# Performance work log

Hardware: AMD Instinct MI355X
Metric: run time of the kernel (lower is better)

## Reference

```python
import jax, jax.numpy as jnp
import numpy as np

# Dims: B=batch, C=n_car, N=n_node, E=embed_dim, H=n_heads
B, C, N, E = 64, 8, 512, 512
H = 8
CLIP = 10.0


def setup_inputs() -> dict:
    key = jax.random.key(0)
    ks = jax.random.split(key, 12)
    s = 1.0 / np.sqrt(E)
    mask = jax.random.bernoulli(ks[10], 0.3, (B, C, 1, N))
    mask = mask.at[..., 0].set(False)  # ensure at least one unmasked node per (b,c)
    return {
        "node_embeddings": jax.random.normal(ks[0], (B, N, E), jnp.float32),
        "graph_embedding": jax.random.normal(ks[1], (B, E), jnp.float32),
        "step_context": jax.random.normal(ks[2], (B, C, 1, E + 2), jnp.float32),
        "mask": mask,
        "Wk1": jax.random.normal(ks[3], (E, E), jnp.float32) * s,
        "Wv": jax.random.normal(ks[4], (E, E), jnp.float32) * s,
        "Wk2": jax.random.normal(ks[5], (E, E), jnp.float32) * s,
        "Wq_fixed": jax.random.normal(ks[6], (E, E), jnp.float32) * s,
        "Wout": jax.random.normal(ks[7], (E, E), jnp.float32) * s,
        "Wq_step": jax.random.normal(ks[8], (E, E + 2), jnp.float32) * s,
        "v": jax.random.uniform(ks[9], (E,), jnp.float32, -s, s),
    }


def reference(node_embeddings, graph_embedding, step_context, mask,
              Wk1, Wv, Wk2, Wq_fixed, Wout, Wq_step, v):
    dh = E // H
    neg = jnp.asarray(-1e9, node_embeddings.dtype)

    # compute_static: projections (torch Linear: x @ W.T). K/V/Q_fixed are
    # broadcast over the car dim instead of materialized via .repeat (same math).
    Q_fixed = (graph_embedding @ Wq_fixed.T)[:, None, None, :]  # [B,1,1,E]
    K1 = node_embeddings @ Wk1.T                                 # [B,N,E]
    V = node_embeddings @ Wv.T                                   # [B,N,E]
    K2 = node_embeddings @ Wk2.T                                 # [B,N,E]

    # compute_dynamic
    Q_step = step_context @ Wq_step.T                            # [B,C,1,E]
    Q1 = Q_fixed + Q_step                                        # [B,C,1,E]

    # MHA (need_W=False): split heads, masked scaled dot-product, merge heads.
    qh = Q1.reshape(B, C, H, dh)                                 # q-len 1 squeezed
    kh = K1.reshape(B, N, H, dh)
    vh = V.reshape(B, N, H, dh)
    scores = jnp.einsum('bchd,bnhd->bchn', qh, kh) * (1.0 / np.sqrt(dh))
    m = mask[:, :, 0, :][:, :, None, :]                          # [B,C,1,N]
    scores = jnp.where(m, neg, scores)
    attn = jax.nn.softmax(scores, axis=-1)
    heads = jnp.einsum('bchn,bnhd->bchd', attn, vh).reshape(B, C, E)
    Q3 = heads @ Wout.T                                          # [B,C,E] (Q2.squeeze(2))

    # Pointer logits (SHA): u = tanh(Q_fixed+Q_step) @ v, repeated over E,
    # dotted with K2 => u_scalar * sum_e K2, then tanh-clipped and masked.
    u_scalar = jnp.einsum('bcqe,e->bcq', jnp.tanh(Q1), v)        # [B,C,1]
    k2sum = K2.sum(-1)                                           # [B,N]
    raw = u_scalar * k2sum[:, None, :]                           # [B,C,N]
    logits = CLIP * jnp.tanh(raw * (1.0 / np.sqrt(E)))
    logits = jnp.where(mask[:, :, 0, :], neg, logits)
    logits = logits.reshape(B, C * N)                            # view(batch, -1)
    return logits, Q3
```

## Files before the change

kernel.cpp:

```cpp
#include <hip/hip_runtime.h>


typedef _Float16 f16x8 __attribute__((ext_vector_type(8)));
typedef float f32x4 __attribute__((ext_vector_type(4)));

__device__ __forceinline__ void async16(const void* g, void* l) {
  __builtin_amdgcn_global_load_lds(
      (const __attribute__((address_space(1))) unsigned int*)g,
      (__attribute__((address_space(3))) unsigned int*)l, 16, 0, 0);
}

__global__ __launch_bounds__(256) void prep_w(const float* __restrict__ Wk1,
                                              const float* __restrict__ Wv,
                                              const float* __restrict__ Wk2,
                                              _Float16* __restrict__ W1h,
                                              _Float16* __restrict__ W2h,
                                              float* __restrict__ colsum) {
  const int bid = blockIdx.x;
  if (bid < 16) {
    const int tx = threadIdx.x & 31, ty = threadIdx.x >> 5;
    const int col = bid * 32 + tx;
    float s = 0.f;
#pragma unroll 4
    for (int e = ty * 64; e < ty * 64 + 64; ++e) s += Wk2[e * 512 + col];
    __shared__ float red[8][32];
    red[ty][tx] = s;
    __syncthreads();
    if (ty == 0) {
      float t = 0.f;
#pragma unroll
      for (int g = 0; g < 8; ++g) t += red[g][tx];
      colsum[col] = t;
    }
  } else {
    const int cb = bid - 16;
    const float* src = (cb < 128) ? Wk1 : Wv;
    _Float16* dst = (cb < 128) ? W1h : W2h;
    const size_t off = (size_t)(cb & 127) * 2048 + threadIdx.x * 8;
    float4 a = *(const float4*)(src + off);
    float4 b = *(const float4*)(src + off + 4);
    union { _Float16 h[8]; uint4 u; } pk;
    pk.h[0] = (_Float16)a.x; pk.h[1] = (_Float16)a.y;
    pk.h[2] = (_Float16)a.z; pk.h[3] = (_Float16)a.w;
    pk.h[4] = (_Float16)b.x; pk.h[5] = (_Float16)b.y;
    pk.h[6] = (_Float16)b.z; pk.h[7] = (_Float16)b.w;
    *(uint4*)(dst + off) = pk.u;
  }
}

__global__ __launch_bounds__(256) void q1_mfma_kernel(
    const float* __restrict__ ge, const float* __restrict__ sc,
    const float* __restrict__ Wqf, const float* __restrict__ Wqs,
    float* __restrict__ Q1) {
  const int mb = blockIdx.x, nb = blockIdx.y, ks = blockIdx.z;
  const int tid = threadIdx.x;
  const int lane = tid & 63, wave = tid >> 6;
  const int wm = (wave >> 1) * 32, wn = (wave & 1) * 32;

  __shared__ __align__(16) _Float16 As[64][40];
  __shared__ __align__(16) _Float16 Ws[64][40];

  f32x4 acc[2][2] = {};
  const int qd = (lane >> 4) * 8, rr = lane & 15;

  for (int kt = 0; kt < 9; ++kt) {
    const int kb = ks * 288 + kt * 32;
#pragma unroll
    for (int f0 = 0; f0 < 2; ++f0) {
      int f = tid + f0 * 256;
      int r = f >> 3, c4 = (f & 7) * 4;
      int m = mb * 64 + r;
      int e = nb * 64 + r;
#pragma unroll
      for (int j = 0; j < 4; ++j) {
        int k = kb + c4 + j;
        float a = 0.f, w = 0.f;
        if (k < 512) {
          a = ge[(m >> 3) * 512 + k];
          w = Wqf[(size_t)e * 512 + k];
        } else if (k < 1026) {
          a = sc[(size_t)m * 514 + (k - 512)];
          w = Wqs[(size_t)e * 514 + (k - 512)];
        }
        As[r][c4 + j] = (_Float16)a;
        Ws[r][c4 + j] = (_Float16)w;
      }
    }
    __syncthreads();
    f16x8 af[2], bfr[2];
#pragma unroll
    for (int mi = 0; mi < 2; ++mi) af[mi] = *(const f16x8*)&As[wm + mi * 16 + rr][qd];
#pragma unroll
    for (int ni = 0; ni < 2; ++ni) bfr[ni] = *(const f16x8*)&Ws[wn + ni * 16 + rr][qd];
#pragma unroll
    for (int mi = 0; mi < 2; ++mi)
#pragma unroll
      for (int ni = 0; ni < 2; ++ni)
        acc[mi][ni] =
            __builtin_amdgcn_mfma_f32_16x16x32_f16(af[mi], bfr[ni], acc[mi][ni], 0, 0, 0);
    __syncthreads();
  }

  const int col = lane & 15, rq = (lane >> 4) * 4;
#pragma unroll
  for (int mi = 0; mi < 2; ++mi)
#pragma unroll
    for (int ni = 0; ni < 2; ++ni)
#pragma unroll
      for (int r = 0; r < 4; ++r) {
        int m = mb * 64 + wm + mi * 16 + rq + r;
        int e = nb * 64 + wn + ni * 16 + col;
        atomicAdd(&Q1[(size_t)m * 512 + e], acc[mi][ni][r]);
      }
}

__global__ __launch_bounds__(256, 2) void gemm_kv(
    const float* __restrict__ A, const _Float16* __restrict__ W1,
    const _Float16* __restrict__ W2, const float* __restrict__ colsum,
    _Float16* __restrict__ K1, _Float16* __restrict__ Vt,
    float* __restrict__ k2sum) {
  const int flat = (int)(blockIdx.y * 4 + blockIdx.x);
  const int work = (flat & 7) * 128 + (flat >> 3);
  const int nb = work & 3;
  const int mb = work >> 2;
  const int tid = threadIdx.x, lane = tid & 63, wave = tid >> 6;
  const int wm = (wave >> 1) * 64, wn = (wave & 1) * 64;
  const int row0 = mb * 128, col0 = nb * 128;
  const int b = mb >> 2;

  __shared__ __align__(16) _Float16 Ah[128 * 64];
  __shared__ __align__(16) _Float16 Wb[2][2][128 * 64];

  f32x4 acc1[4][4] = {}, acc2[4][4] = {};
  float k2p[4] = {0.f, 0.f, 0.f, 0.f};
  const int q = lane >> 4, rr = lane & 15;
  const int wlr = lane >> 3, wlc = lane & 7;
  const int cswz = wlc ^ wlr;

  const int ar0 = tid >> 3, ac = tid & 7;
  const float* aptr = A + (size_t)(row0 + ar0) * 512 + ac * 8;
  const int aslot = ac ^ (ar0 & 7);

  float4 areg[4][2];
  float4 cs0, cs1;

  auto issue_a = [&](int kt) {
#pragma unroll
    for (int j = 0; j < 4; ++j) {
      const float* gp = aptr + (size_t)j * 32 * 512 + kt * 64;
      areg[j][0] = *(const float4*)gp;
      areg[j][1] = *(const float4*)(gp + 4);
    }
    if (nb == 0) {
      const float* csp = colsum + kt * 64 + ac * 8;
      cs0 = *(const float4*)csp;
      cs1 = *(const float4*)(csp + 4);
    }
  };
  auto issue_w = [&](int kt, int buf) {
    const int kbase = kt * 64;
#pragma unroll
    for (int j = 0; j < 4; ++j) {
      int r = wave * 32 + j * 8 + wlr;
      int ldsrow = (wave * 32 + j * 8) * 64;
      size_t goff = (size_t)(col0 + r) * 512 + kbase + cswz * 8;
      async16(W1 + goff, &Wb[buf][0][ldsrow]);
      async16(W2 + goff, &Wb[buf][1][ldsrow]);
    }
  };
  auto write_a = [&](int kt) {
#pragma unroll
    for (int j = 0; j < 4; ++j) {
      union { _Float16 h[8]; uint4 u; } pk;
      float4 lo = areg[j][0], hi = areg[j][1];
      pk.h[0] = (_Float16)lo.x; pk.h[1] = (_Float16)lo.y;
      pk.h[2] = (_Float16)lo.z; pk.h[3] = (_Float16)lo.w;
      pk.h[4] = (_Float16)hi.x; pk.h[5] = (_Float16)hi.y;
      pk.h[6] = (_Float16)hi.z; pk.h[7] = (_Float16)hi.w;
      *(uint4*)&Ah[(ar0 + 32 * j) * 64 + aslot * 8] = pk.u;
    }
    if (nb == 0) {
#pragma unroll
      for (int j = 0; j < 4; ++j) {
        float4 lo = areg[j][0], hi = areg[j][1];
        k2p[j] += lo.x * cs0.x + lo.y * cs0.y + lo.z * cs0.z + lo.w * cs0.w +
                  hi.x * cs1.x + hi.y * cs1.y + hi.z * cs1.z + hi.w * cs1.w;
      }
    }
  };

  issue_a(0);
  issue_w(0, 0);
  write_a(0);
  __syncthreads();

  for (int kt = 0; kt < 8; ++kt) {
    const int p = kt & 1;
    if (kt < 7) {
      issue_a(kt + 1);
      issue_w(kt + 1, p ^ 1);
    }
#pragma unroll
    for (int k0 = 0; k0 < 64; k0 += 32) {
      const int cb = (k0 >> 3) + q;
      f16x8 af[4], b1[4], b2[4];
#pragma unroll
      for (int mi = 0; mi < 4; ++mi) {
        int ra = wm + mi * 16 + rr;
        af[mi] = *(const f16x8*)&Ah[ra * 64 + (cb ^ (ra & 7)) * 8];
      }
#pragma unroll
      for (int ni = 0; ni < 4; ++ni) {
        int rw = wn + ni * 16 + rr;
        int slot = cb ^ (rw & 7);
        b1[ni] = *(const f16x8*)&Wb[p][0][rw * 64 + slot * 8];
        b2[ni] = *(const f16x8*)&Wb[p][1][rw * 64 + slot * 8];
      }
      __builtin_amdgcn_s_setprio(1);
#pragma unroll
      for (int mi = 0; mi < 4; ++mi)
#pragma unroll
        for (int ni = 0; ni < 4; ++ni) {
          acc1[mi][ni] =
              __builtin_amdgcn_mfma_f32_16x16x32_f16(af[mi], b1[ni], acc1[mi][ni], 0, 0, 0);
          acc2[mi][ni] =
              __builtin_amdgcn_mfma_f32_16x16x32_f16(af[mi], b2[ni], acc2[mi][ni], 0, 0, 0);
        }
      __builtin_amdgcn_s_setprio(0);
    }
    if (kt < 7) {
      __syncthreads();
      write_a(kt + 1);
      __syncthreads();
    }
  }

  if (nb == 0) {
#pragma unroll
    for (int j = 0; j < 4; ++j) {
      float s = k2p[j];
      s += __shfl_xor(s, 1, 8);
      s += __shfl_xor(s, 2, 8);
      s += __shfl_xor(s, 4, 8);
      if (ac == 0) k2sum[row0 + ar0 + 32 * j] = s;
    }
  }

  const int col = lane & 15, rq = (lane >> 4) * 4;
#pragma unroll
  for (int mi = 0; mi < 4; ++mi)
#pragma unroll
    for (int ni = 0; ni < 4; ++ni)
#pragma unroll
      for (int r = 0; r < 4; ++r) {
        size_t m = row0 + wm + mi * 16 + rq + r;
        size_t e = col0 + wn + ni * 16 + col;
        K1[m * 512 + e] = (_Float16)acc1[mi][ni][r];
      }

  _Float16* Vts = &Wb[0][0][0];
#pragma unroll
  for (int mi = 0; mi < 4; ++mi)
#pragma unroll
    for (int ni = 0; ni < 4; ++ni) {
      int n0 = wm + mi * 16 + rq;
      int el = wn + ni * 16 + col;
      int cn = n0 >> 3, half = (n0 >> 2) & 1;
      int slot = cn ^ (el & 7);
      union { _Float16 h[4]; unsigned long long u; } pk;
#pragma unroll
      for (int r = 0; r < 4; ++r) pk.h[r] = (_Float16)acc2[mi][ni][r];
      *(unsigned long long*)&Vts[el * 128 + slot * 8 + half * 4] = pk.u;
    }
  __syncthreads();
  const int nbase = row0 & 511;
#pragma unroll
  for (int i = 0; i < 8; ++i) {
    int f = tid + i * 256;
    int el = f >> 4, c16 = f & 15;
    int slot = c16 ^ (el & 7);
    uint4 val = *(const uint4*)&Vts[el * 128 + slot * 8];
    *(uint4*)(Vt + (size_t)b * 262144 + (size_t)(col0 + el) * 512 + nbase + c16 * 8) = val;
  }
}

__global__ __launch_bounds__(256) void attn_kernel(
    const float* __restrict__ Q1, const _Float16* __restrict__ K1,
    const _Float16* __restrict__ Vt, const int* __restrict__ mask,
    float* __restrict__ heads) {
  const int bid = blockIdx.x;
  const int b = bid >> 3, h = bid & 7;
  const int tid = threadIdx.x, wave = tid >> 6, lane = tid & 63;
  const int q = lane >> 4, cl = lane & 15;

  __shared__ __align__(16) _Float16 kt[256 * 64];
  __shared__ __align__(16) _Float16 P[16][520];
  __shared__ float red[4][8];

  f16x8 af[2];
  {
    const float* qp = Q1 + (size_t)(b * 8 + (cl & 7)) * 512 + h * 64 + q * 8;
#pragma unroll
    for (int s = 0; s < 2; ++s) {
      float4 l0 = *(const float4*)(qp + s * 32);
      float4 l1 = *(const float4*)(qp + s * 32 + 4);
      af[s][0] = (_Float16)l0.x; af[s][1] = (_Float16)l0.y;
      af[s][2] = (_Float16)l0.z; af[s][3] = (_Float16)l0.w;
      af[s][4] = (_Float16)l1.x; af[s][5] = (_Float16)l1.y;
      af[s][6] = (_Float16)l1.z; af[s][7] = (_Float16)l1.w;
    }
  }

  f32x4 acc[8] = {};
  const _Float16* Kb = K1 + (size_t)b * 262144 + h * 64;
  for (int h2 = 0; h2 < 2; ++h2) {
#pragma unroll
    for (int j = 0; j < 8; ++j) {
      int r = wave * 64 + j * 8 + (lane >> 3);
      int cg = (lane & 7) ^ (r & 7);
      async16(Kb + (size_t)(h2 * 256 + r) * 512 + cg * 8, &kt[(wave * 64 + j * 8) * 64]);
    }
    __syncthreads();
    __builtin_amdgcn_s_setprio(1);
#pragma unroll
    for (int tt = 0; tt < 4; ++tt) {
      int rn = wave * 64 + tt * 16 + cl;
#pragma unroll
      for (int s = 0; s < 2; ++s) {
        int slot = (s * 4 + q) ^ (cl & 7);
        f16x8 bf = *(const f16x8*)&kt[rn * 64 + slot * 8];
        acc[h2 * 4 + tt] =
            __builtin_amdgcn_mfma_f32_16x16x32_f16(af[s], bf, acc[h2 * 4 + tt], 0, 0, 0);
      }
    }
    __builtin_amdgcn_s_setprio(0);
    __syncthreads();
  }

  const _Float16* Vb = Vt + (size_t)b * 262144 + (size_t)h * 64 * 512;
#pragma unroll
  for (int j = 0; j < 8; ++j) {
    int r = wave * 16 + j * 2 + (lane >> 5);
    int cg = (lane & 31) ^ (r & 7);
    async16(Vb + (size_t)r * 512 + cg * 8, &kt[(wave * 16 + j * 2) * 256]);
  }

  float gmax[4], rsum[4];
  if (q < 2) {
    float mx[4] = {-3e38f, -3e38f, -3e38f, -3e38f};
#pragma unroll
    for (int t = 0; t < 8; ++t) {
      int n = (t >> 2) * 256 + wave * 64 + (t & 3) * 16 + cl;
#pragma unroll
      for (int r = 0; r < 4; ++r) {
        int c = q * 4 + r;
        float x = mask[(size_t)(b * 8 + c) * 512 + n] ? -1e9f : acc[t][r] * 0.125f;
        acc[t][r] = x;
        mx[r] = fmaxf(mx[r], x);
      }
    }
#pragma unroll
    for (int off = 1; off < 16; off <<= 1)
#pragma unroll
      for (int r = 0; r < 4; ++r) mx[r] = fmaxf(mx[r], __shfl_xor(mx[r], off, 64));
    if (cl == 0)
#pragma unroll
      for (int r = 0; r < 4; ++r) red[wave][q * 4 + r] = mx[r];
  }
  __syncthreads();
  if (q < 2) {
#pragma unroll
    for (int r = 0; r < 4; ++r) {
      int c = q * 4 + r;
      gmax[r] = fmaxf(fmaxf(red[0][c], red[1][c]), fmaxf(red[2][c], red[3][c]));
    }
  }
  __syncthreads();
  if (q < 2) {
#pragma unroll
    for (int r = 0; r < 4; ++r) rsum[r] = 0.f;
#pragma unroll
    for (int t = 0; t < 8; ++t) {
      int n = (t >> 2) * 256 + wave * 64 + (t & 3) * 16 + cl;
#pragma unroll
      for (int r = 0; r < 4; ++r) {
        float e = __expf(acc[t][r] - gmax[r]);
        rsum[r] += e;
        P[q * 4 + r][n] = (_Float16)e;
      }
    }
#pragma unroll
    for (int off = 1; off < 16; off <<= 1)
#pragma unroll
      for (int r = 0; r < 4; ++r) rsum[r] += __shfl_xor(rsum[r], off, 64);
    if (cl == 0)
#pragma unroll
      for (int r = 0; r < 4; ++r) red[wave][q * 4 + r] = rsum[r];
  }
  __syncthreads();

  f32x4 pacc = {};
  const int rn = wave * 16 + cl;
  __builtin_amdgcn_s_setprio(1);
#pragma unroll
  for (int sl = 0; sl < 8; ++sl) {
    int slot = (sl * 4 + q) ^ (cl & 7);
    f16x8 bf = *(const f16x8*)&kt[rn * 256 + slot * 8];
    f16x8 pa = *(const f16x8*)&P[cl][sl * 32 + q * 8];
    pacc = __builtin_amdgcn_mfma_f32_16x16x32_f16(pa, bf, pacc, 0, 0, 0);
  }
  __builtin_amdgcn_s_setprio(0);
  __syncthreads();
#pragma unroll
  for (int j = 0; j < 8; ++j) {
    int r = wave * 16 + j * 2 + (lane >> 5);
    int cg = (lane & 31) ^ (r & 7);
    async16(Vb + (size_t)r * 512 + 256 + cg * 8, &kt[(wave * 16 + j * 2) * 256]);
  }
  __syncthreads();
  __builtin_amdgcn_s_setprio(1);
#pragma unroll
  for (int sl = 0; sl < 8; ++sl) {
    int slot = (sl * 4 + q) ^ (cl & 7);
    f16x8 bf = *(const f16x8*)&kt[rn * 256 + slot * 8];
    f16x8 pa = *(const f16x8*)&P[cl][256 + sl * 32 + q * 8];
    pacc = __builtin_amdgcn_mfma_f32_16x16x32_f16(pa, bf, pacc, 0, 0, 0);
  }
  __builtin_amdgcn_s_setprio(0);

  if (q < 2) {
#pragma unroll
    for (int r = 0; r < 4; ++r) {
      int c = q * 4 + r;
      float inv = 1.f / (red[0][c] + red[1][c] + red[2][c] + red[3][c]);
      heads[(size_t)(b * 8 + c) * 512 + h * 64 + wave * 16 + cl] = pacc[r] * inv;
    }
  }
}

__global__ __launch_bounds__(256) void gemm_out64(const float* __restrict__ A,
                                                  const float* __restrict__ W,
                                                  float* __restrict__ C) {
  const int mb = blockIdx.x, nb = blockIdx.y, ks = blockIdx.z;
  const int tid = threadIdx.x;
  const int lane = tid & 63, wave = tid >> 6;
  const int wm = (wave >> 1) * 32, wn = (wave & 1) * 32;

  __shared__ __align__(16) _Float16 As[64][40];
  __shared__ __align__(16) _Float16 Ws[64][40];

  f32x4 acc[2][2] = {};
  const int qd = (lane >> 4) * 8, rr = lane & 15;

  for (int kt = 0; kt < 8; ++kt) {
    const int kb = ks * 256 + kt * 32;
#pragma unroll
    for (int f0 = 0; f0 < 2; ++f0) {
      int f = tid + f0 * 256;
      int r = f >> 3, c4 = (f & 7) * 4;
      float4 a = *(const float4*)(A + (size_t)(mb * 64 + r) * 512 + kb + c4);
      float4 w = *(const float4*)(W + (size_t)(nb * 64 + r) * 512 + kb + c4);
      As[r][c4 + 0] = (_Float16)a.x; As[r][c4 + 1] = (_Float16)a.y;
      As[r][c4 + 2] = (_Float16)a.z; As[r][c4 + 3] = (_Float16)a.w;
      Ws[r][c4 + 0] = (_Float16)w.x; Ws[r][c4 + 1] = (_Float16)w.y;
      Ws[r][c4 + 2] = (_Float16)w.z; Ws[r][c4 + 3] = (_Float16)w.w;
    }
    __syncthreads();
    f16x8 af[2], bfr[2];
#pragma unroll
    for (int mi = 0; mi < 2; ++mi) af[mi] = *(const f16x8*)&As[wm + mi * 16 + rr][qd];
#pragma unroll
    for (int ni = 0; ni < 2; ++ni) bfr[ni] = *(const f16x8*)&Ws[wn + ni * 16 + rr][qd];
#pragma unroll
    for (int mi = 0; mi < 2; ++mi)
#pragma unroll
      for (int ni = 0; ni < 2; ++ni)
        acc[mi][ni] =
            __builtin_amdgcn_mfma_f32_16x16x32_f16(af[mi], bfr[ni], acc[mi][ni], 0, 0, 0);
    __syncthreads();
  }

  const int col = lane & 15, rq = (lane >> 4) * 4;
#pragma unroll
  for (int mi = 0; mi < 2; ++mi)
#pragma unroll
    for (int ni = 0; ni < 2; ++ni)
#pragma unroll
      for (int r = 0; r < 4; ++r) {
        int m = mb * 64 + wm + mi * 16 + rq + r;
        int e = nb * 64 + wn + ni * 16 + col;
        atomicAdd(&C[(size_t)m * 512 + e], acc[mi][ni][r]);
      }
}

__global__ __launch_bounds__(256) void logits_u_kernel(
    const float* __restrict__ Q1, const float* __restrict__ v,
    const float* __restrict__ k2s, const int* __restrict__ mask,
    float* __restrict__ out) {
  const int bc = blockIdx.x;
  const int b = bc >> 3;
  const int tid = threadIdx.x;
  const int wave = tid >> 6, lane = tid & 63;

  float p = tanhf(Q1[(size_t)bc * 512 + tid]) * v[tid] +
            tanhf(Q1[(size_t)bc * 512 + tid + 256]) * v[tid + 256];
#pragma unroll
  for (int off = 32; off; off >>= 1) p += __shfl_down(p, off, 64);
  __shared__ float red[4];
  __shared__ float su;
  if (lane == 0) red[wave] = p;
  __syncthreads();
  if (tid == 0) su = red[0] + red[1] + red[2] + red[3];
  __syncthreads();
  const float u = su;

#pragma unroll
  for (int i = 0; i < 2; ++i) {
    int n = tid + i * 256;
    int idx = bc * 512 + n;
    out[idx] = mask[idx] ? -1e9f
                         : 10.f * tanhf(u * k2s[b * 512 + n] * 0.04419417382415922f);
  }
}

extern "C" void kernel_launch(void* const* d_in, const int* in_sizes, int n_in,
                              void* d_out, int out_size, void* d_ws, size_t ws_size,
                              hipStream_t stream) {
  const float* ne = (const float*)d_in[0];
  const float* ge = (const float*)d_in[1];
  const float* sc = (const float*)d_in[2];
  const int* mask = (const int*)d_in[3];
  const float* Wk1 = (const float*)d_in[4];
  const float* Wv = (const float*)d_in[5];
  const float* Wk2 = (const float*)d_in[6];
  const float* Wqf = (const float*)d_in[7];
  const float* Wout = (const float*)d_in[8];
  const float* Wqs = (const float*)d_in[9];
  const float* v = (const float*)d_in[10];

  float* logits = (float*)d_out;
  float* q3 = (float*)d_out + 262144;

  char* ws = (char*)d_ws;
  _Float16* K1 = (_Float16*)(ws + 0);
  _Float16* Vt = (_Float16*)(ws + 33554432);
  float* Q1 = (float*)(ws + 67108864);
  float* heads = (float*)(ws + 68157440);
  float* k2sum = (float*)(ws + 69206016);
  float* colsum = (float*)(ws + 69337088);
  _Float16* W1h = (_Float16*)(ws + 69339136);
  _Float16* W2h = (_Float16*)(ws + 69863424);

  hipMemsetAsync(Q1, 0, 1048576, stream);
  hipMemsetAsync(q3, 0, 1048576, stream);
  prep_w<<<272, 256, 0, stream>>>(Wk1, Wv, Wk2, W1h, W2h, colsum);
  q1_mfma_kernel<<<dim3(8, 8, 4), 256, 0, stream>>>(ge, sc, Wqf, Wqs, Q1);
  gemm_kv<<<dim3(4, 256), 256, 0, stream>>>(ne, W1h, W2h, colsum, K1, Vt, k2sum);
  attn_kernel<<<512, 256, 0, stream>>>(Q1, K1, Vt, mask, heads);
  gemm_out64<<<dim3(8, 8, 2), 256, 0, stream>>>(heads, Wout, q3);
  logits_u_kernel<<<512, 256, 0, stream>>>(Q1, v, k2sum, mask, logits);
}
```

Before: 216.8 us.

## Split fused K1/V GEMM into separate passes to raise occupancy

The fused gemm_kv kernel, which computed K1 and V together from one shared A tile, is split into two block types, each computing a single output (K1 or V). This halves the accumulator registers and the W shared-memory buffers per block, and launch bounds rise to 3 blocks per CU, with 2048 blocks instead of 1024. In exchange, each A tile is now loaded from global memory and converted to fp16 twice, once per pass. The k2sum reduction moves to only the pass-0 nb-0 blocks.

```diff
diff --git a/kernel.cpp b/kernel.cpp
--- a/kernel.cpp
+++ b/kernel.cpp
@@ -114,24 +114,29 @@
       }
 }
 
-__global__ __launch_bounds__(256, 2) void gemm_kv(
+__global__ __launch_bounds__(256, 3) void gemm_kv(
     const float* __restrict__ A, const _Float16* __restrict__ W1,
     const _Float16* __restrict__ W2, const float* __restrict__ colsum,
     _Float16* __restrict__ K1, _Float16* __restrict__ Vt,
     float* __restrict__ k2sum) {
-  const int flat = (int)(blockIdx.y * 4 + blockIdx.x);
-  const int work = (flat & 7) * 128 + (flat >> 3);
+  const int flat = (int)blockIdx.x;
+  const int work = (flat & 7) * 256 + (flat >> 3);
+  const int mb = work >> 3;
+  const int pass = (work >> 2) & 1;
   const int nb = work & 3;
-  const int mb = work >> 2;
+  const bool do_k2 = (work & 7) == 0;
   const int tid = threadIdx.x, lane = tid & 63, wave = tid >> 6;
   const int wm = (wave >> 1) * 64, wn = (wave & 1) * 64;
   const int row0 = mb * 128, col0 = nb * 128;
   const int b = mb >> 2;
 
-  __shared__ __align__(16) _Float16 Ah[128 * 64];
-  __shared__ __align__(16) _Float16 Wb[2][2][128 * 64];
-
-  f32x4 acc1[4][4] = {}, acc2[4][4] = {};
+  __shared__ __align__(16) _Float16 S[24576];
+  _Float16* Ah = S;
+  _Float16* Wb = S + 8192;
+
+  const _Float16* W = pass ? W2 : W1;
+
+  f32x4 acc[4][4] = {};
   float k2p[4] = {0.f, 0.f, 0.f, 0.f};
   const int q = lane >> 4, rr = lane & 15;
   const int wlr = lane >> 3, wlc = lane & 7;
@@ -151,7 +156,7 @@
       areg[j][0] = *(const float4*)gp;
       areg[j][1] = *(const float4*)(gp + 4);
     }
-    if (nb == 0) {
+    if (do_k2) {
       const float* csp = colsum + kt * 64 + ac * 8;
       cs0 = *(const float4*)csp;
       cs1 = *(const float4*)(csp + 4);
@@ -164,8 +169,7 @@
       int r = wave * 32 + j * 8 + wlr;
       int ldsrow = (wave * 32 + j * 8) * 64;
       size_t goff = (size_t)(col0 + r) * 512 + kbase + cswz * 8;
-      async16(W1 + goff, &Wb[buf][0][ldsrow]);
-      async16(W2 + goff, &Wb[buf][1][ldsrow]);
+      async16(W + goff, Wb + buf * 8192 + ldsrow);
     }
   };
   auto write_a = [&](int kt) {
@@ -179,7 +183,7 @@
       pk.h[6] = (_Float16)hi.z; pk.h[7] = (_Float16)hi.w;
       *(uint4*)&Ah[(ar0 + 32 * j) * 64 + aslot * 8] = pk.u;
     }
-    if (nb == 0) {
+    if (do_k2) {
 #pragma unroll
       for (int j = 0; j < 4; ++j) {
         float4 lo = areg[j][0], hi = areg[j][1];
@@ -203,7 +207,7 @@
 #pragma unroll
     for (int k0 = 0; k0 < 64; k0 += 32) {
       const int cb = (k0 >> 3) + q;
-      f16x8 af[4], b1[4], b2[4];
+      f16x8 af[4], bf[4];
 #pragma unroll
       for (int mi = 0; mi < 4; ++mi) {
         int ra = wm + mi * 16 + rr;
@@ -213,19 +217,15 @@
       for (int ni = 0; ni < 4; ++ni) {
         int rw = wn + ni * 16 + rr;
         int slot = cb ^ (rw & 7);
-        b1[ni] = *(const f16x8*)&Wb[p][0][rw * 64 + slot * 8];
-        b2[ni] = *(const f16x8*)&Wb[p][1][rw * 64 + slot * 8];
+        bf[ni] = *(const f16x8*)&Wb[p * 8192 + rw * 64 + slot * 8];
       }
       __builtin_amdgcn_s_setprio(1);
 #pragma unroll
       for (int mi = 0; mi < 4; ++mi)
 #pragma unroll
-        for (int ni = 0; ni < 4; ++ni) {
-          acc1[mi][ni] =
-              __builtin_amdgcn_mfma_f32_16x16x32_f16(af[mi], b1[ni], acc1[mi][ni], 0, 0, 0);
-          acc2[mi][ni] =
-              __builtin_amdgcn_mfma_f32_16x16x32_f16(af[mi], b2[ni], acc2[mi][ni], 0, 0, 0);
-        }
+        for (int ni = 0; ni < 4; ++ni)
+          acc[mi][ni] =
+              __builtin_amdgcn_mfma_f32_16x16x32_f16(af[mi], bf[ni], acc[mi][ni], 0, 0, 0);
       __builtin_amdgcn_s_setprio(0);
     }
     if (kt < 7) {
@@ -235,52 +235,55 @@
     }
   }
 
-  if (nb == 0) {
-#pragma unroll
-    for (int j = 0; j < 4; ++j) {
-      float s = k2p[j];
-      s += __shfl_xor(s, 1, 8);
-      s += __shfl_xor(s, 2, 8);
-      s += __shfl_xor(s, 4, 8);
-      if (ac == 0) k2sum[row0 + ar0 + 32 * j] = s;
-    }
-  }
-
   const int col = lane & 15, rq = (lane >> 4) * 4;
-#pragma unroll
-  for (int mi = 0; mi < 4; ++mi)
-#pragma unroll
-    for (int ni = 0; ni < 4; ++ni)
-#pragma unroll
-      for (int r = 0; r < 4; ++r) {
-        size_t m = row0 + wm + mi * 16 + rq + r;
-        size_t e = col0 + wn + ni * 16 + col;
-        K1[m * 512 + e] = (_Float16)acc1[mi][ni][r];
-      }
-
-  _Float16* Vts = &Wb[0][0][0];
-#pragma unroll
-  for (int mi = 0; mi < 4; ++mi)
-#pragma unroll
-    for (int ni = 0; ni < 4; ++ni) {
-      int n0 = wm + mi * 16 + rq;
-      int el = wn + ni * 16 + col;
-      int cn = n0 >> 3, half = (n0 >> 2) & 1;
-      int slot = cn ^ (el & 7);
-      union { _Float16 h[4]; unsigned long long u; } pk;
-#pragma unroll
-      for (int r = 0; r < 4; ++r) pk.h[r] = (_Float16)acc2[mi][ni][r];
-      *(unsigned long long*)&Vts[el * 128 + slot * 8 + half * 4] = pk.u;
-    }
-  __syncthreads();
-  const int nbase = row0 & 511;
-#pragma unroll
-  for (int i = 0; i < 8; ++i) {
-    int f = tid + i * 256;
-    int el = f >> 4, c16 = f & 15;
-    int slot = c16 ^ (el & 7);
-    uint4 val = *(const uint4*)&Vts[el * 128 + slot * 8];
-    *(uint4*)(Vt + (size_t)b * 262144 + (size_t)(col0 + el) * 512 + nbase + c16 * 8) = val;
+
+  if (pass == 0) {
+    if (do_k2) {
+#pragma unroll
+      for (int j = 0; j < 4; ++j) {
+        float s = k2p[j];
+        s += __shfl_xor(s, 1, 8);
+        s += __shfl_xor(s, 2, 8);
+        s += __shfl_xor(s, 4, 8);
+        if (ac == 0) k2sum[row0 + ar0 + 32 * j] = s;
+      }
+    }
+#pragma unroll
+    for (int mi = 0; mi < 4; ++mi)
+#pragma unroll
+      for (int ni = 0; ni < 4; ++ni)
+#pragma unroll
+        for (int r = 0; r < 4; ++r) {
+          size_t m = row0 + wm + mi * 16 + rq + r;
+          size_t e = col0 + wn + ni * 16 + col;
+          K1[m * 512 + e] = (_Float16)acc[mi][ni][r];
+        }
+  } else {
+    __syncthreads();
+    _Float16* Vts = S;
+#pragma unroll
+    for (int mi = 0; mi < 4; ++mi)
+#pragma unroll
+      for (int ni = 0; ni < 4; ++ni) {
+        int n0 = wm + mi * 16 + rq;
+        int el = wn + ni * 16 + col;
+        int cn = n0 >> 3, half = (n0 >> 2) & 1;
+        int slot = cn ^ (el & 7);
+        union { _Float16 h[4]; unsigned long long u; } pk;
+#pragma unroll
+        for (int r = 0; r < 4; ++r) pk.h[r] = (_Float16)acc[mi][ni][r];
+        *(unsigned long long*)&Vts[el * 128 + slot * 8 + half * 4] = pk.u;
+      }
+    __syncthreads();
+    const int nbase = row0 & 511;
+#pragma unroll
+    for (int i = 0; i < 8; ++i) {
+      int f = tid + i * 256;
+      int el = f >> 4, c16 = f & 15;
+      int slot = c16 ^ (el & 7);
+      uint4 val = *(const uint4*)&Vts[el * 128 + slot * 8];
+      *(uint4*)(Vt + (size_t)b * 262144 + (size_t)(col0 + el) * 512 + nbase + c16 * 8) = val;
+    }
   }
 }
 
@@ -555,7 +558,7 @@
   hipMemsetAsync(q3, 0, 1048576, stream);
   prep_w<<<272, 256, 0, stream>>>(Wk1, Wv, Wk2, W1h, W2h, colsum);
   q1_mfma_kernel<<<dim3(8, 8, 4), 256, 0, stream>>>(ge, sc, Wqf, Wqs, Q1);
-  gemm_kv<<<dim3(4, 256), 256, 0, stream>>>(ne, W1h, W2h, colsum, K1, Vt, k2sum);
+  gemm_kv<<<2048, 256, 0, stream>>>(ne, W1h, W2h, colsum, K1, Vt, k2sum);
   attn_kernel<<<512, 256, 0, stream>>>(Q1, K1, Vt, mask, heads);
   gemm_out64<<<dim3(8, 8, 2), 256, 0, stream>>>(heads, Wout, q3);
   logits_u_kernel<<<512, 256, 0, stream>>>(Q1, v, k2sum, mask, logits);
```

Result: slower. 225.3 us (+3.9%).

## Merge independent kernels into combined launches and use fast tanh

Applied to the files above, without the earlier changes.

Fuses prep_w with the Q1 projection kernel, and the output GEMM with the logits kernel, into single launches that branch on block index. This removes two kernel launches and their tail gaps. The output GEMM split-K factor goes from 2 to 4, which adds parallelism at the cost of more atomics. tanhf is replaced by an exp-based fast_tanh. It also changes the k2sum row index expression, which may be a fix or a cosmetic change.

```diff
diff --git a/kernel.cpp b/kernel.cpp
--- a/kernel.cpp
+++ b/kernel.cpp
@@ -10,49 +10,56 @@
       (__attribute__((address_space(3))) unsigned int*)l, 16, 0, 0);
 }
 
-__global__ __launch_bounds__(256) void prep_w(const float* __restrict__ Wk1,
-                                              const float* __restrict__ Wv,
-                                              const float* __restrict__ Wk2,
-                                              _Float16* __restrict__ W1h,
-                                              _Float16* __restrict__ W2h,
-                                              float* __restrict__ colsum) {
-  const int bid = blockIdx.x;
-  if (bid < 16) {
-    const int tx = threadIdx.x & 31, ty = threadIdx.x >> 5;
-    const int col = bid * 32 + tx;
-    float s = 0.f;
-#pragma unroll 4
-    for (int e = ty * 64; e < ty * 64 + 64; ++e) s += Wk2[e * 512 + col];
-    __shared__ float red[8][32];
-    red[ty][tx] = s;
-    __syncthreads();
-    if (ty == 0) {
-      float t = 0.f;
-#pragma unroll
-      for (int g = 0; g < 8; ++g) t += red[g][tx];
-      colsum[col] = t;
-    }
-  } else {
-    const int cb = bid - 16;
-    const float* src = (cb < 128) ? Wk1 : Wv;
-    _Float16* dst = (cb < 128) ? W1h : W2h;
-    const size_t off = (size_t)(cb & 127) * 2048 + threadIdx.x * 8;
-    float4 a = *(const float4*)(src + off);
-    float4 b = *(const float4*)(src + off + 4);
-    union { _Float16 h[8]; uint4 u; } pk;
-    pk.h[0] = (_Float16)a.x; pk.h[1] = (_Float16)a.y;
-    pk.h[2] = (_Float16)a.z; pk.h[3] = (_Float16)a.w;
-    pk.h[4] = (_Float16)b.x; pk.h[5] = (_Float16)b.y;
-    pk.h[6] = (_Float16)b.z; pk.h[7] = (_Float16)b.w;
-    *(uint4*)(dst + off) = pk.u;
-  }
-}
-
-__global__ __launch_bounds__(256) void q1_mfma_kernel(
+__device__ __forceinline__ float fast_tanh(float x) {
+  float ax = fabsf(x);
+  float t = __expf(-2.f * ax);
+  float r = (1.f - t) / (1.f + t);
+  return copysignf(r, x);
+}
+
+__global__ __launch_bounds__(256) void prep_q1(
+    const float* __restrict__ Wk1, const float* __restrict__ Wv,
+    const float* __restrict__ Wk2, _Float16* __restrict__ W1h,
+    _Float16* __restrict__ W2h, float* __restrict__ colsum,
     const float* __restrict__ ge, const float* __restrict__ sc,
     const float* __restrict__ Wqf, const float* __restrict__ Wqs,
     float* __restrict__ Q1) {
-  const int mb = blockIdx.x, nb = blockIdx.y, ks = blockIdx.z;
+  const int bid = blockIdx.x;
+  if (bid < 272) {
+    if (bid < 16) {
+      const int tx = threadIdx.x & 31, ty = threadIdx.x >> 5;
+      const int col = bid * 32 + tx;
+      float s = 0.f;
+#pragma unroll 4
+      for (int e = ty * 64; e < ty * 64 + 64; ++e) s += Wk2[e * 512 + col];
+      __shared__ float red[8][32];
+      red[ty][tx] = s;
+      __syncthreads();
+      if (ty == 0) {
+        float t = 0.f;
+#pragma unroll
+        for (int g = 0; g < 8; ++g) t += red[g][tx];
+        colsum[col] = t;
+      }
+    } else {
+      const int cb = bid - 16;
+      const float* src = (cb < 128) ? Wk1 : Wv;
+      _Float16* dst = (cb < 128) ? W1h : W2h;
+      const size_t off = (size_t)(cb & 127) * 2048 + threadIdx.x * 8;
+      float4 a = *(const float4*)(src + off);
+      float4 b = *(const float4*)(src + off + 4);
+      union { _Float16 h[8]; uint4 u; } pk;
+      pk.h[0] = (_Float16)a.x; pk.h[1] = (_Float16)a.y;
+      pk.h[2] = (_Float16)a.z; pk.h[3] = (_Float16)a.w;
+      pk.h[4] = (_Float16)b.x; pk.h[5] = (_Float16)b.y;
+      pk.h[6] = (_Float16)b.z; pk.h[7] = (_Float16)b.w;
+      *(uint4*)(dst + off) = pk.u;
+    }
+    return;
+  }
+
+  const int b2 = bid - 272;
+  const int mb = b2 & 7, nb = (b2 >> 3) & 7, ks = b2 >> 6;
   const int tid = threadIdx.x;
   const int lane = tid & 63, wave = tid >> 6;
   const int wm = (wave >> 1) * 32, wn = (wave & 1) * 32;
@@ -242,7 +249,7 @@
       s += __shfl_xor(s, 1, 8);
       s += __shfl_xor(s, 2, 8);
       s += __shfl_xor(s, 4, 8);
-      if (ac == 0) k2sum[row0 + ar0 + 32 * j] = s;
+      if (ac == 0) k2sum[row0 + (tid >> 3) + 32 * j] = s;
     }
   }
 
@@ -438,72 +445,73 @@
   }
 }
 
-__global__ __launch_bounds__(256) void gemm_out64(const float* __restrict__ A,
-                                                  const float* __restrict__ W,
-                                                  float* __restrict__ C) {
-  const int mb = blockIdx.x, nb = blockIdx.y, ks = blockIdx.z;
-  const int tid = threadIdx.x;
-  const int lane = tid & 63, wave = tid >> 6;
-  const int wm = (wave >> 1) * 32, wn = (wave & 1) * 32;
-
-  __shared__ __align__(16) _Float16 As[64][40];
-  __shared__ __align__(16) _Float16 Ws[64][40];
-
-  f32x4 acc[2][2] = {};
-  const int qd = (lane >> 4) * 8, rr = lane & 15;
-
-  for (int kt = 0; kt < 8; ++kt) {
-    const int kb = ks * 256 + kt * 32;
-#pragma unroll
-    for (int f0 = 0; f0 < 2; ++f0) {
-      int f = tid + f0 * 256;
-      int r = f >> 3, c4 = (f & 7) * 4;
-      float4 a = *(const float4*)(A + (size_t)(mb * 64 + r) * 512 + kb + c4);
-      float4 w = *(const float4*)(W + (size_t)(nb * 64 + r) * 512 + kb + c4);
-      As[r][c4 + 0] = (_Float16)a.x; As[r][c4 + 1] = (_Float16)a.y;
-      As[r][c4 + 2] = (_Float16)a.z; As[r][c4 + 3] = (_Float16)a.w;
-      Ws[r][c4 + 0] = (_Float16)w.x; Ws[r][c4 + 1] = (_Float16)w.y;
-      Ws[r][c4 + 2] = (_Float16)w.z; Ws[r][c4 + 3] = (_Float16)w.w;
-    }
-    __syncthreads();
-    f16x8 af[2], bfr[2];
-#pragma unroll
-    for (int mi = 0; mi < 2; ++mi) af[mi] = *(const f16x8*)&As[wm + mi * 16 + rr][qd];
-#pragma unroll
-    for (int ni = 0; ni < 2; ++ni) bfr[ni] = *(const f16x8*)&Ws[wn + ni * 16 + rr][qd];
+__global__ __launch_bounds__(256) void out_logits(
+    const float* __restrict__ A, const float* __restrict__ W,
+    float* __restrict__ C, const float* __restrict__ Q1,
+    const float* __restrict__ v, const float* __restrict__ k2s,
+    const int* __restrict__ mask, float* __restrict__ out) {
+  const int bid = blockIdx.x;
+  if (bid < 256) {
+    const int mb = bid & 7, nb = (bid >> 3) & 7, ks = bid >> 6;
+    const int tid = threadIdx.x;
+    const int lane = tid & 63, wave = tid >> 6;
+    const int wm = (wave >> 1) * 32, wn = (wave & 1) * 32;
+
+    __shared__ __align__(16) _Float16 As[64][40];
+    __shared__ __align__(16) _Float16 Ws[64][40];
+
+    f32x4 acc[2][2] = {};
+    const int qd = (lane >> 4) * 8, rr = lane & 15;
+
+    for (int kt = 0; kt < 4; ++kt) {
+      const int kb = ks * 128 + kt * 32;
+#pragma unroll
+      for (int f0 = 0; f0 < 2; ++f0) {
+        int f = tid + f0 * 256;
+        int r = f >> 3, c4 = (f & 7) * 4;
+        float4 a = *(const float4*)(A + (size_t)(mb * 64 + r) * 512 + kb + c4);
+        float4 w = *(const float4*)(W + (size_t)(nb * 64 + r) * 512 + kb + c4);
+        As[r][c4 + 0] = (_Float16)a.x; As[r][c4 + 1] = (_Float16)a.y;
+        As[r][c4 + 2] = (_Float16)a.z; As[r][c4 + 3] = (_Float16)a.w;
+        Ws[r][c4 + 0] = (_Float16)w.x; Ws[r][c4 + 1] = (_Float16)w.y;
+        Ws[r][c4 + 2] = (_Float16)w.z; Ws[r][c4 + 3] = (_Float16)w.w;
+      }
+      __syncthreads();
+      f16x8 af[2], bfr[2];
+#pragma unroll
+      for (int mi = 0; mi < 2; ++mi) af[mi] = *(const f16x8*)&As[wm + mi * 16 + rr][qd];
+#pragma unroll
+      for (int ni = 0; ni < 2; ++ni) bfr[ni] = *(const f16x8*)&Ws[wn + ni * 16 + rr][qd];
+#pragma unroll
+      for (int mi = 0; mi < 2; ++mi)
+#pragma unroll
+        for (int ni = 0; ni < 2; ++ni)
+          acc[mi][ni] =
+              __builtin_amdgcn_mfma_f32_16x16x32_f16(af[mi], bfr[ni], acc[mi][ni], 0, 0, 0);
+      __syncthreads();
+    }
+
+    const int col = lane & 15, rq = (lane >> 4) * 4;
 #pragma unroll
     for (int mi = 0; mi < 2; ++mi)
 #pragma unroll
       for (int ni = 0; ni < 2; ++ni)
-        acc[mi][ni] =
-            __builtin_amdgcn_mfma_f32_16x16x32_f16(af[mi], bfr[ni], acc[mi][ni], 0, 0, 0);
-    __syncthreads();
-  }
-
-  const int col = lane & 15, rq = (lane >> 4) * 4;
-#pragma unroll
-  for (int mi = 0; mi < 2; ++mi)
-#pragma unroll
-    for (int ni = 0; ni < 2; ++ni)
-#pragma unroll
-      for (int r = 0; r < 4; ++r) {
-        int m = mb * 64 + wm + mi * 16 + rq + r;
-        int e = nb * 64 + wn + ni * 16 + col;
-        atomicAdd(&C[(size_t)m * 512 + e], acc[mi][ni][r]);
-      }
-}
-
-__global__ __launch_bounds__(256) void logits_u_kernel(
-    const float* __restrict__ Q1, const float* __restrict__ v,
-    const float* __restrict__ k2s, const int* __restrict__ mask,
-    float* __restrict__ out) {
-  const int bc = blockIdx.x;
+#pragma unroll
+        for (int r = 0; r < 4; ++r) {
+          int m = mb * 64 + wm + mi * 16 + rq + r;
+          int e = nb * 64 + wn + ni * 16 + col;
+          atomicAdd(&C[(size_t)m * 512 + e], acc[mi][ni][r]);
+        }
+    return;
+  }
+
+  const int bc = bid - 256;
   const int b = bc >> 3;
   const int tid = threadIdx.x;
   const int wave = tid >> 6, lane = tid & 63;
 
-  float p = tanhf(Q1[(size_t)bc * 512 + tid]) * v[tid] +
-            tanhf(Q1[(size_t)bc * 512 + tid + 256]) * v[tid + 256];
+  float p = fast_tanh(Q1[(size_t)bc * 512 + tid]) * v[tid] +
+            fast_tanh(Q1[(size_t)bc * 512 + tid + 256]) * v[tid + 256];
 #pragma unroll
   for (int off = 32; off; off >>= 1) p += __shfl_down(p, off, 64);
   __shared__ float red[4];
@@ -519,7 +527,7 @@
     int n = tid + i * 256;
     int idx = bc * 512 + n;
     out[idx] = mask[idx] ? -1e9f
-                         : 10.f * tanhf(u * k2s[b * 512 + n] * 0.04419417382415922f);
+                         : 10.f * fast_tanh(u * k2s[b * 512 + n] * 0.04419417382415922f);
   }
 }
 
@@ -553,10 +561,9 @@
 
   hipMemsetAsync(Q1, 0, 1048576, stream);
   hipMemsetAsync(q3, 0, 1048576, stream);
-  prep_w<<<272, 256, 0, stream>>>(Wk1, Wv, Wk2, W1h, W2h, colsum);
-  q1_mfma_kernel<<<dim3(8, 8, 4), 256, 0, stream>>>(ge, sc, Wqf, Wqs, Q1);
+  prep_q1<<<528, 256, 0, stream>>>(Wk1, Wv, Wk2, W1h, W2h, colsum,
+                                   ge, sc, Wqf, Wqs, Q1);
   gemm_kv<<<dim3(4, 256), 256, 0, stream>>>(ne, W1h, W2h, colsum, K1, Vt, k2sum);
   attn_kernel<<<512, 256, 0, stream>>>(Q1, K1, Vt, mask, heads);
-  gemm_out64<<<dim3(8, 8, 2), 256, 0, stream>>>(heads, Wout, q3);
-  logits_u_kernel<<<512, 256, 0, stream>>>(Q1, v, k2sum, mask, logits);
-}
+  out_logits<<<768, 256, 0, stream>>>(heads, Wout, q3, Q1, v, k2sum, mask, logits);
+}
```

After: 204.3 us. -5.8%, faster.
